# Optimization experiments

Hardware: AMD Instinct MI355X
Metric: run time of the kernel (lower is better)

Reference implementation:

```python
import jax, jax.numpy as jnp
import numpy as np

N = 50000          # nodes
E = 800000         # edges (avg degree 16)
IN, H, OUT = 128, 256, 128
K = 100            # low-rank attention rank (hard-coded self.k = 100)
BN_EPS = 1e-5


def _lin(key, din, dout):
    return jax.random.normal(key, (din, dout), jnp.float32) / np.sqrt(din)


def setup_inputs() -> dict:
    key = jax.random.key(0)
    ks = jax.random.split(key, 16)
    inp = {
        "x": jax.random.normal(ks[0], (N, IN), jnp.float32),
        "edge_index": jax.random.randint(ks[1], (2, E), 0, N, jnp.int32),
    }
    dins = [IN, H, H]
    douts = [H, H, OUT]
    j = 2
    for i, (di, do) in enumerate(zip(dins, douts)):
        inp[f"cw{i}"] = _lin(ks[j], di, H); j += 1          # GCNConv weight
        inp[f"cb{i}"] = jnp.zeros((H,), jnp.float32)          # GCNConv bias
        inp[f"aw{i}"] = _lin(ks[j], di, 4 * K); j += 1        # attention U|V|Z|T projection
        inp[f"ab{i}"] = jnp.zeros((4 * K,), jnp.float32)
        inp[f"rw{i}"] = _lin(ks[j], 2 * K + H, do); j += 1    # dimension_reduce linear
        inp[f"rb{i}"] = jnp.zeros((do,), jnp.float32)
    for i in range(2):                                        # BN for first num_layers-1 blocks
        inp[f"g{i}"] = jnp.ones((H,), jnp.float32)
        inp[f"bt{i}"] = jnp.zeros((H,), jnp.float32)
    return inp


def _gcn(x, W, b, src, dst):
    n = x.shape[0]
    loops = jnp.arange(n, dtype=src.dtype)
    s = jnp.concatenate([src, loops])
    d = jnp.concatenate([dst, loops])
    deg = jax.ops.segment_sum(jnp.ones(d.shape, x.dtype), d, num_segments=n)
    dis = jax.lax.rsqrt(jnp.maximum(deg, 1.0))  # deg >= 1 due to self loops
    h = x @ W                                    # [N, H]
    msg = h[s] * (dis[s] * dis[d])[:, None]      # [E+N, H]
    return jax.ops.segment_sum(msg, d, num_segments=n) + b


def _lowrank(x, Aw, Ab):
    # LowRankAttention: tmp = relu(x W); split into U,V,Z,T of width K each.
    t = jax.nn.relu(x @ Aw + Ab)                 # [N, 4K]
    U, V, Z, T = t[:, :K], t[:, K:2 * K], t[:, 2 * K:3 * K], t[:, 3 * K:]
    n = x.shape[0]
    # joint_normalize2: scalar norm factor
    nf = jnp.sum(U @ (V.T @ jnp.ones((n, 1), x.dtype))) / n + 1e-6
    res = U @ (V.T @ Z)                          # low-rank global attention [N, K]
    return jnp.concatenate([res / nf, T], axis=1)  # [N, 2K]


def _bn(x, g, b):
    m = jnp.mean(x, axis=0)
    v = jnp.var(x, axis=0)
    return (x - m) * jax.lax.rsqrt(v + BN_EPS) * g + b


def reference(x, edge_index, cw0, cb0, aw0, ab0, rw0, rb0, g0, bt0,
              cw1, cb1, aw1, ab1, rw1, rb1, g1, bt1,
              cw2, cb2, aw2, ab2, rw2, rb2):
    src, dst = edge_index[0], edge_index[1]
    layers = [(cw0, cb0, aw0, ab0, rw0, rb0, g0, bt0),
              (cw1, cb1, aw1, ab1, rw1, rb1, g1, bt1)]
    for cw, cb, aw, ab, rw, rb, g, bt in layers:
        x_local = jax.nn.relu(_gcn(x, cw, cb, src, dst))  # dropout p=0 (eval)
        x_global = _lowrank(x, aw, ab)
        x = jax.nn.relu(jnp.concatenate([x_global, x_local], axis=1) @ rw + rb)
        x = _bn(x, g, bt)
    x_local = jax.nn.relu(_gcn(x, cw2, cb2, src, dst))
    x_global = _lowrank(x, aw2, ab2)
    return jnp.concatenate([x_global, x_local], axis=1) @ rw2 + rb2
```

## Files before the change

### kernel.cpp

```cpp
#include <hip/hip_runtime.h>

typedef _Float16 f16;
typedef __attribute__((ext_vector_type(8))) _Float16 f16x8;
typedef __attribute__((ext_vector_type(4))) _Float16 f16x4;
typedef __attribute__((ext_vector_type(2))) _Float16 f16x2;
typedef __attribute__((ext_vector_type(4))) float f32x4;

__global__ __launch_bounds__(256, 4) void gemm4(
    const f16* __restrict__ A, int lda,
    const f16* __restrict__ Bt, int Kd,
    const float* __restrict__ bias,
    f16* __restrict__ Cb, float* __restrict__ Cf, int ldc,
    int R, int ncols, int relu,
    float* __restrict__ csbuf,
    float* __restrict__ bnsum_ptr,
    f16* __restrict__ hbD, f16* __restrict__ tbufD, f16* __restrict__ xcatD,
    int mode)
{
    __shared__ char smem[36864];
    f16* As = (f16*)smem;
    f16* Bs = (f16*)(smem + 18432);
    float* scr = (float*)(smem + 34816);

    const int tid  = threadIdx.x;
    const int wid  = tid >> 6;
    const int lane = tid & 63;
    const int m    = lane & 15;
    const int quad = lane >> 4;
    const int wr   = wid >> 1;
    const int wc   = wid & 1;

    const long rowblk  = (long)blockIdx.x * 128;
    const int  colbase = blockIdx.y * 128;

    f32x4 acc[4][4];
#pragma unroll
    for (int rt = 0; rt < 4; ++rt)
#pragma unroll
        for (int ct = 0; ct < 4; ++ct)
            acc[rt][ct] = f32x4{0.f, 0.f, 0.f, 0.f};

    for (int k0 = 0; k0 < Kd; k0 += 64) {
        const int BK = (Kd - k0 >= 64) ? 64 : (Kd - k0);
        if (k0) __syncthreads();
        if (BK == 64) {
#pragma unroll
            for (int i = 0; i < 4; ++i) {
                int u = i * 256 + tid;
                int r = u >> 3, s = u & 7;
                long rr = rowblk + r; if (rr > (long)R - 1) rr = (long)R - 1;
                *(f16x8*)&As[r * 72 + s * 8] = *(const f16x8*)(A + rr * (long)lda + k0 + s * 8);
            }
#pragma unroll
            for (int i = 0; i < 4; ++i) {
                int u = i * 256 + tid;
                int c = u >> 3, s = u & 7;
                *(f16x8*)&Bs[c * 72 + s * 8] =
                    *(const f16x8*)(Bt + (long)(colbase + c) * Kd + k0 + s * 8);
            }
        } else {
#pragma unroll
            for (int i = 0; i < 2; ++i) {
                int u = i * 256 + tid;
                int r = u >> 2, s = u & 3;
                long rr = rowblk + r; if (rr > (long)R - 1) rr = (long)R - 1;
                *(f16x8*)&As[r * 72 + s * 8] = *(const f16x8*)(A + rr * (long)lda + k0 + s * 8);
            }
#pragma unroll
            for (int i = 0; i < 2; ++i) {
                int u = i * 256 + tid;
                int c = u >> 2, s = u & 3;
                *(f16x8*)&Bs[c * 72 + s * 8] =
                    *(const f16x8*)(Bt + (long)(colbase + c) * Kd + k0 + s * 8);
            }
        }
        __syncthreads();
#pragma unroll 2
        for (int kk = 0; kk < BK; kk += 32) {
            f16x8 a[4], b[4];
#pragma unroll
            for (int rt = 0; rt < 4; ++rt)
                a[rt] = *(const f16x8*)&As[(wr * 64 + rt * 16 + m) * 72 + kk + quad * 8];
#pragma unroll
            for (int ct = 0; ct < 4; ++ct)
                b[ct] = *(const f16x8*)&Bs[(wc * 64 + ct * 16 + m) * 72 + kk + quad * 8];
#pragma unroll
            for (int ct = 0; ct < 4; ++ct)
#pragma unroll
                for (int rt = 0; rt < 4; ++rt)
                    acc[rt][ct] = __builtin_amdgcn_mfma_f32_16x16x32_f16(a[rt], b[ct], acc[rt][ct], 0, 0, 0);
        }
    }

    __syncthreads();

    if (mode == 0 && Cf) {
#pragma unroll
        for (int ct = 0; ct < 4; ++ct) {
            int col = colbase + wc * 64 + ct * 16 + m;
            if (col >= ncols) continue;
            float bv = bias ? bias[col] : 0.f;
#pragma unroll
            for (int rt = 0; rt < 4; ++rt) {
#pragma unroll
                for (int r = 0; r < 4; ++r) {
                    long row = rowblk + wr * 64 + rt * 16 + quad * 4 + r;
                    if (row < R) {
                        float v = acc[rt][ct][r] + bv;
                        if (relu && v < 0.f) v = 0.f;
                        Cf[row * (long)ldc + col] = v;
                    }
                }
            }
        }
        return;
    }

    float rsum[4], rsq[4];
#pragma unroll
    for (int ct = 0; ct < 4; ++ct) { rsum[ct] = 0.f; rsq[ct] = 0.f; }

    f16* epw = (f16*)smem + wid * (64 * 68);

    const bool needsum = (mode == 1) ? (colbase == 256 || colbase == 384)
                                     : (bnsum_ptr != nullptr);

#pragma unroll
    for (int ct = 0; ct < 4; ++ct) {
        int col = colbase + wc * 64 + ct * 16 + m;
        float bv;
        if (mode == 1) bv = bias[col];
        else           bv = (bias && col < ncols) ? bias[col] : 0.f;
        bool isrelu = (mode == 1) ? (col >= 256) : (relu != 0);
#pragma unroll
        for (int rt = 0; rt < 4; ++rt) {
#pragma unroll
            for (int r = 0; r < 4; ++r) {
                long row = rowblk + wr * 64 + rt * 16 + quad * 4 + r;
                float v = acc[rt][ct][r] + bv;
                if (isrelu && v < 0.f) v = 0.f;
                if (needsum && row < R && col < ((mode == 1) ? 656 : ncols)) {
                    rsum[ct] += v;
                    rsq[ct]  += v * v;
                }
                epw[(rt * 16 + quad * 4 + r) * 68 + ct * 16 + m] = (f16)v;
            }
        }
    }

#pragma unroll
    for (int it = 0; it < 16; ++it) {
        int rl = it * 4 + (lane >> 4);
        int ch = lane & 15;
        long grow = rowblk + wr * 64 + rl;
        if (grow >= R) continue;
        f16x4 vv = *(const f16x4*)&epw[rl * 68 + ch * 4];
        int c4 = colbase + wc * 64 + ch * 4;
        if (mode == 1) {
            f16* dst; int ld2, c2;
            if (c4 < 256)      { dst = hbD;   ld2 = 256; c2 = c4; }
            else if (c4 < 556) { dst = tbufD; ld2 = 300; c2 = c4 - 256; }
            else if (c4 < 656) { dst = xcatD; ld2 = 456; c2 = c4 - 556; }
            else continue;
            *(f16x4*)&dst[grow * (long)ld2 + c2] = vv;
        } else {
            if (c4 < ncols)
                *(f16x4*)&Cb[grow * (long)ldc + c4] = vv;
        }
    }

    if (needsum) {
        __syncthreads();
#pragma unroll
        for (int ct = 0; ct < 4; ++ct) {
            float s = rsum[ct];
            s += __shfl_xor(s, 16);
            s += __shfl_xor(s, 32);
            float q = rsq[ct];
            q += __shfl_xor(q, 16);
            q += __shfl_xor(q, 32);
            if (quad == 0) {
                scr[wr * 128 + wc * 64 + ct * 16 + m]       = s;
                scr[256 + wr * 128 + wc * 64 + ct * 16 + m] = q;
            }
        }
        __syncthreads();
        if (tid < 128) {
            int gcol = colbase + tid;
            float s = scr[tid] + scr[128 + tid];
            if (mode == 1) {
                if (gcol >= 256 && gcol < 456) atomicAdd(&csbuf[gcol - 256], s);
            } else if (gcol < ncols) {
                float q = scr[256 + tid] + scr[384 + tid];
                atomicAdd(&bnsum_ptr[gcol], s);
                atomicAdd(&bnsum_ptr[256 + gcol], q);
            }
        }
    }
}

struct PrepJobs {
    const float* src[13];
    void*        dst[13];
    int   K[13], ncols[13], Kd[13], type[13];
    long  start[13], elems[13];
    int   njobs;
};

__global__ __launch_bounds__(256) void prep_all(PrepJobs J)
{
    long b = blockIdx.x;
    int j = 0;
    for (int i = 1; i < J.njobs; ++i)
        if (b >= J.start[i]) j = i;
    long idx = (b - J.start[j]) * 256 + threadIdx.x;
    if (idx >= J.elems[j]) return;
    int ty = J.type[j];
    if (ty == 0) {
        int Kd = J.Kd[j];
        int k = (int)(idx % Kd);
        long n = idx / Kd;
        float v = (k < J.K[j] && n < J.ncols[j]) ? J.src[j][(long)k * J.ncols[j] + n] : 0.f;
        ((f16*)J.dst[j])[idx] = (f16)v;
    } else if (ty == 1) {
        ((f16*)J.dst[j])[idx] = (f16)J.src[j][idx];
    } else if (ty == 2) {
        ((float*)J.dst[j])[idx] = 0.f;
    } else {
        float v = (idx >= 256 && idx < 656) ? J.src[j][idx - 256] : 0.f;
        ((float*)J.dst[j])[idx] = v;
    }
}

__global__ void hist_kernel(const int* __restrict__ dst, int E, int* __restrict__ cnt)
{
    int e = blockIdx.x * 256 + threadIdx.x;
    if (e < E) atomicAdd(&cnt[dst[e]], 1);
}

__global__ __launch_bounds__(1024) void scanA_kernel(const int* __restrict__ cnt, int n,
                                                     int* __restrict__ csum)
{
    __shared__ int sdata[1024];
    int t = threadIdx.x;
    int i = blockIdx.x * 1024 + t;
    sdata[t] = (i < n) ? cnt[i] : 0;
    __syncthreads();
    for (int d = 512; d > 0; d >>= 1) {
        if (t < d) sdata[t] += sdata[t + d];
        __syncthreads();
    }
    if (t == 0) csum[blockIdx.x] = sdata[0];
}

__global__ void scanB_kernel(int* __restrict__ csum, int nchunks, int n, int* __restrict__ rowptr)
{
    if (threadIdx.x == 0) {
        int run = 0;
        for (int b = 0; b < nchunks; ++b) {
            int v = csum[b];
            csum[b] = run;
            run += v;
        }
        rowptr[n] = run;
    }
}

__global__ __launch_bounds__(1024) void scanC_kernel(const int* __restrict__ cnt, int n,
                                                     const int* __restrict__ csum,
                                                     int* __restrict__ rowptr,
                                                     int* __restrict__ cursor,
                                                     float* __restrict__ dis)
{
    __shared__ int sdata[1024];
    int t = threadIdx.x;
    int i = blockIdx.x * 1024 + t;
    int v = (i < n) ? cnt[i] : 0;
    sdata[t] = v;
    __syncthreads();
    for (int d = 1; d < 1024; d <<= 1) {
        int x = (t >= d) ? sdata[t - d] : 0;
        __syncthreads();
        sdata[t] += x;
        __syncthreads();
    }
    if (i < n) {
        int excl = csum[blockIdx.x] + sdata[t] - v;
        rowptr[i] = excl;
        cursor[i] = excl;
        dis[i] = rsqrtf((float)(v + 1));
    }
}

__global__ void scatter_kernel(const int* __restrict__ src, const int* __restrict__ dst,
                               int E, int* __restrict__ cursor, int* __restrict__ colidx)
{
    int e = blockIdx.x * 256 + threadIdx.x;
    if (e < E) {
        int d = dst[e];
        int pos = atomicAdd(&cursor[d], 1);
        colidx[pos] = src[e];
    }
}

__global__ __launch_bounds__(256) void agg_kernel(
    const f16* __restrict__ h, const int* __restrict__ rowptr,
    const int* __restrict__ colidx, const float* __restrict__ dis,
    const float* __restrict__ cb, f16* __restrict__ out, int ldc, int R)
{
    int wid = threadIdx.x >> 6, lane = threadIdx.x & 63;
    int i = blockIdx.x * 4 + wid;
    if (i >= R) return;
    float disi = dis[i];
    f16x4 hv = *(const f16x4*)(h + (long)i * 256 + lane * 4);
    float acc[4];
#pragma unroll
    for (int j = 0; j < 4; ++j) acc[j] = (float)hv[j] * disi;
    int e0 = rowptr[i], e1 = rowptr[i + 1];
    int e = e0;
    for (; e + 3 < e1; e += 4) {
        int s0 = colidx[e], s1 = colidx[e + 1], s2 = colidx[e + 2], s3 = colidx[e + 3];
        float w0 = dis[s0], w1 = dis[s1], w2 = dis[s2], w3 = dis[s3];
        f16x4 h0 = *(const f16x4*)(h + (long)s0 * 256 + lane * 4);
        f16x4 h1 = *(const f16x4*)(h + (long)s1 * 256 + lane * 4);
        f16x4 h2 = *(const f16x4*)(h + (long)s2 * 256 + lane * 4);
        f16x4 h3 = *(const f16x4*)(h + (long)s3 * 256 + lane * 4);
#pragma unroll
        for (int j = 0; j < 4; ++j)
            acc[j] += (float)h0[j] * w0 + (float)h1[j] * w1
                    + (float)h2[j] * w2 + (float)h3[j] * w3;
    }
    for (; e < e1; ++e) {
        int s = colidx[e];
        float w = dis[s];
        f16x4 hs = *(const f16x4*)(h + (long)s * 256 + lane * 4);
#pragma unroll
        for (int j = 0; j < 4; ++j) acc[j] += (float)hs[j] * w;
    }
    f16x4 o;
#pragma unroll
    for (int j = 0; j < 4; ++j) {
        float v = acc[j] * disi + cb[lane * 4 + j];
        if (v < 0.f) v = 0.f;
        o[j] = (f16)v;
    }
    *(f16x4*)(out + (long)i * ldc + lane * 4) = o;
}

#define VTZ_BLOCKS 192
__global__ __launch_bounds__(256) void vtz_mfma(const f16* __restrict__ t, int ld, int R,
                                                float* __restrict__ Mpart)
{
    __shared__ f16 Vt[112 * 72];
    __shared__ f16 Zt[112 * 72];
    const int tid  = threadIdx.x;
    const int wid  = tid >> 6;
    const int lane = tid & 63;
    const int m    = lane & 15;
    const int quad = lane >> 4;

    for (int idx = tid; idx < 12 * 64; idx += 256) {
        int c = 100 + (idx >> 6), r = idx & 63;
        Vt[c * 72 + r] = (f16)0.f;
        Zt[c * 72 + r] = (f16)0.f;
    }

    f32x4 acc[2][7];
#pragma unroll
    for (int rt = 0; rt < 2; ++rt)
#pragma unroll
        for (int ct = 0; ct < 7; ++ct)
            acc[rt][ct] = f32x4{0.f, 0.f, 0.f, 0.f};

    for (long base = (long)blockIdx.x * 64; base < R; base += (long)gridDim.x * 64) {
        __syncthreads();
        for (int idx = tid; idx < 50 * 64; idx += 256) {
            int r = idx / 50, c2 = (idx - r * 50) * 2;
            f16x2 v2 = f16x2{(f16)0.f, (f16)0.f};
            f16x2 z2 = f16x2{(f16)0.f, (f16)0.f};
            if (base + r < R) {
                v2 = *(const f16x2*)(t + (base + r) * ld + 100 + c2);
                z2 = *(const f16x2*)(t + (base + r) * ld + 200 + c2);
            }
            Vt[c2 * 72 + r] = v2[0]; Vt[(c2 + 1) * 72 + r] = v2[1];
            Zt[c2 * 72 + r] = z2[0]; Zt[(c2 + 1) * 72 + r] = z2[1];
        }
        __syncthreads();
#pragma unroll
        for (int ks = 0; ks < 2; ++ks) {
            int k0 = ks * 32 + quad * 8;
            f16x8 b[7];
#pragma unroll
            for (int ct = 0; ct < 7; ++ct)
                b[ct] = *(const f16x8*)&Zt[(ct * 16 + m) * 72 + k0];
#pragma unroll
            for (int rt = 0; rt < 2; ++rt) {
                int tr = wid + rt * 4;
                if (tr >= 7) continue;
                f16x8 a = *(const f16x8*)&Vt[(tr * 16 + m) * 72 + k0];
#pragma unroll
                for (int ct = 0; ct < 7; ++ct)
                    acc[rt][ct] = __builtin_amdgcn_mfma_f32_16x16x32_f16(a, b[ct], acc[rt][ct], 0, 0, 0);
            }
        }
    }

    float* out = Mpart + (long)blockIdx.x * 10000;
#pragma unroll
    for (int rt = 0; rt < 2; ++rt) {
        int tr = wid + rt * 4;
        if (tr >= 7) continue;
#pragma unroll
        for (int ct = 0; ct < 7; ++ct) {
            int b = ct * 16 + m;
            if (b >= 100) continue;
#pragma unroll
            for (int r = 0; r < 4; ++r) {
                int a = tr * 16 + quad * 4 + r;
                if (a < 100) out[a * 100 + b] = acc[rt][ct][r];
            }
        }
    }
}

__global__ __launch_bounds__(256) void vtz_reduce2(const float* __restrict__ Mpart,
                                                   f16* __restrict__ MT,
                                                   const float* __restrict__ cs, int R)
{
    __shared__ float s2[256];
    int t = threadIdx.x;
    float v = (t < 100) ? cs[t] * cs[100 + t] : 0.f;
    s2[t] = v;
    __syncthreads();
    for (int d = 128; d > 0; d >>= 1) {
        if (t < d) s2[t] += s2[t + d];
        __syncthreads();
    }
    float scale = 1.0f / (s2[0] / (float)R + 1e-6f);

    int idx = blockIdx.x * 256 + t;
    if (idx >= 10000) return;
    float s = 0.f;
    for (int b = 0; b < VTZ_BLOCKS; ++b) s += Mpart[(long)b * 10000 + idx];
    s *= scale;
    int a = idx / 100, c = idx - a * 100;
    MT[c * 128 + a] = (f16)s;
}

__global__ __launch_bounds__(256) void bn_fold2(
    f16* __restrict__ bigBT,
    const float* __restrict__ cwf, const float* __restrict__ awf,
    const float* __restrict__ bnsum, const float* __restrict__ g,
    const float* __restrict__ bt, int R,
    const float* __restrict__ ab0, float* __restrict__ biascat)
{
    __shared__ float a_s[256], b_s[256];
    const int t = threadIdx.x;
    {
        float s0 = bnsum[t];
        float s1 = bnsum[256 + t];
        float mean = s0 / (float)R;
        float var  = s1 / (float)R - mean * mean;
        if (var < 0.f) var = 0.f;
        float a = g[t] * rsqrtf(var + 1e-5f);
        a_s[t] = a;
        b_s[t] = bt[t] - mean * a;
    }
    __syncthreads();
    const int bid = blockIdx.x;
    if (bid < 768) {
        long idx = (long)bid * 256 + t;
        bigBT[idx] = (f16)((float)bigBT[idx] * a_s[t]);
    } else if (bid == 768) {
        float s = 0.f;
        for (int k = 0; k < 256; ++k) s += b_s[k] * cwf[(long)k * 256 + t];
        biascat[t] = s;
    } else {
        int n = (bid - 769) * 256 + t;
        if (n < 400) {
            float s = ab0[n];
            for (int k = 0; k < 256; ++k) s += b_s[k] * awf[(long)k * 400 + n];
            biascat[256 + n] = s;
        }
    }
}

extern "C" void kernel_launch(void* const* d_in, const int* in_sizes, int n_in,
                              void* d_out, int out_size, void* d_ws, size_t ws_size,
                              hipStream_t stream)
{
    (void)n_in; (void)out_size; (void)ws_size;
    const int N = in_sizes[0] / 128;
    const int E = in_sizes[1] / 2;

    const float* x0 = (const float*)d_in[0];
    const int*  ei   = (const int*)d_in[1];
    const int*  esrc = ei;
    const int*  edst = ei + E;
    const float *cw[3], *cbv[3], *aw[3], *abv[3], *rw[3], *rbv[3];
    for (int l = 0; l < 3; ++l) {
        cw[l]  = (const float*)d_in[2 + 6 * l];
        cbv[l] = (const float*)d_in[3 + 6 * l];
        aw[l]  = (const float*)d_in[4 + 6 * l];
        abv[l] = (const float*)d_in[5 + 6 * l];
        rw[l]  = (const float*)d_in[6 + 6 * l];
        rbv[l] = (const float*)d_in[7 + 6 * l];
    }
    const float* g[2]   = {(const float*)d_in[20], (const float*)d_in[22]};
    const float* btb[2] = {(const float*)d_in[21], (const float*)d_in[23]};

    char* p = (char*)d_ws;
    auto carve = [&](size_t bytes) -> char* {
        char* r = p; p += (bytes + 255) & ~(size_t)255; return r;
    };
    int*   cnt    = (int*)carve((size_t)N * 4);
    int*   rowptr = (int*)carve((size_t)(N + 1) * 4);
    int*   cursor = (int*)carve((size_t)N * 4);
    int*   colidx = (int*)carve((size_t)E * 4);
    float* dis    = (float*)carve((size_t)N * 4);
    int*   csum   = (int*)carve(256 * 4);
    float* Mpart  = (float*)carve((size_t)VTZ_BLOCKS * 10000 * 4);
    float* zr     = (float*)carve(9984 * 4);
    float* csbufL[3] = {zr, zr + 256, zr + 512};
    float* bnsumA = zr + 768;
    float* bnsumB = zr + 1280;
    f16*   MT     = (f16*)(zr + 1792);
    float* biascat = (float*)carve(768 * 4);
    f16*   bigBT[3], *rwT[3];
    int din[3] = {128, 256, 256};
    int dou[3] = {256, 256, 128};
    for (int l = 0; l < 3; ++l) {
        bigBT[l] = (f16*)carve((size_t)768 * din[l] * 2);
        rwT[l]   = (f16*)carve((size_t)dou[l] * 480 * 2);
    }
    f16*   xbf  = (f16*)carve((size_t)N * 256 * 2);
    float* hbuf = (float*)carve((size_t)N * 256 * 4);
    f16*   hb   = (f16*)hbuf;
    f16*   tbuf = (f16*)carve((size_t)N * 300 * 2);
    f16*   xcat = (f16*)carve(((size_t)N * 456 + 32) * 2);

    PrepJobs J{};
    int nj = 0; long blk = 0;
    auto addJob = [&](const float* s, void* d, int K, int nc, int Kd, int ty, long elems) {
        J.src[nj] = s; J.dst[nj] = d; J.K[nj] = K; J.ncols[nj] = nc; J.Kd[nj] = Kd;
        J.type[nj] = ty; J.start[nj] = blk; J.elems[nj] = elems;
        blk += (elems + 255) / 256; ++nj;
    };
    for (int l = 0; l < 3; ++l)
        addJob(cw[l], bigBT[l], din[l], 256, din[l], 0, (long)256 * din[l]);
    for (int l = 0; l < 3; ++l)
        addJob(aw[l], bigBT[l] + (long)256 * din[l], din[l], 400, din[l], 0, (long)512 * din[l]);
    for (int l = 0; l < 3; ++l)
        addJob(rw[l], rwT[l], 456, dou[l], 480, 0, (long)dou[l] * 480);
    addJob(x0, xbf, 0, 0, 0, 1, (long)N * 128);
    addJob(nullptr, zr, 0, 0, 0, 2, 9984);
    addJob(nullptr, cnt, 0, 0, 0, 2, N);
    addJob(abv[0], biascat, 0, 0, 0, 3, 768);
    J.njobs = nj;

    prep_all<<<(unsigned)blk, 256, 0, stream>>>(J);

    const int nchunks = (N + 1023) / 1024;
    hist_kernel<<<(E + 255) / 256, 256, 0, stream>>>(edst, E, cnt);
    scanA_kernel<<<nchunks, 1024, 0, stream>>>(cnt, N, csum);
    scanB_kernel<<<1, 64, 0, stream>>>(csum, nchunks, N, rowptr);
    scanC_kernel<<<nchunks, 1024, 0, stream>>>(cnt, N, csum, rowptr, cursor, dis);
    scatter_kernel<<<(E + 255) / 256, 256, 0, stream>>>(esrc, edst, E, cursor, colidx);

    int lda = 128;
    const unsigned gx = (unsigned)((N + 127) / 128);

    for (int l = 0; l < 3; ++l) {
        float* bnsumX = (l == 0) ? bnsumA : bnsumB;

        gemm4<<<dim3(gx, 6), 256, 0, stream>>>(xbf, lda, bigBT[l], din[l], biascat,
                                               nullptr, nullptr, 0, N, 656, 0,
                                               csbufL[l], nullptr,
                                               hb, tbuf, xcat + 100, 1);
        vtz_mfma<<<VTZ_BLOCKS, 256, 0, stream>>>(tbuf, 300, N, Mpart);
        vtz_reduce2<<<40, 256, 0, stream>>>(Mpart, MT, csbufL[l], N);
        gemm4<<<dim3(gx, 1), 256, 0, stream>>>(tbuf, 300, MT, 128, nullptr,
                                               xcat, nullptr, 456, N, 100, 0,
                                               nullptr, nullptr,
                                               nullptr, nullptr, nullptr, 0);
        agg_kernel<<<(N + 3) / 4, 256, 0, stream>>>(hb, rowptr, colidx, dis, cbv[l],
                                                    xcat + 200, 456, N);
        if (l < 2) {
            gemm4<<<dim3(gx, 2), 256, 0, stream>>>(xcat, 456, rwT[l], 480, rbv[l],
                                                   xbf, nullptr, 256, N, 256, 1,
                                                   nullptr, bnsumX,
                                                   nullptr, nullptr, nullptr, 0);
            bn_fold2<<<771, 256, 0, stream>>>(bigBT[l + 1], cw[l + 1], aw[l + 1],
                                              bnsumX, g[l], btb[l], N,
                                              abv[l + 1], biascat);
            lda = 256;
        } else {
            gemm4<<<dim3(gx, 1), 256, 0, stream>>>(xcat, 456, rwT[l], 480, rbv[l],
                                                   nullptr, (float*)d_out, 128, N, 128, 0,
                                                   nullptr, nullptr,
                                                   nullptr, nullptr, nullptr, 0);
        }
    }
}
```

Baseline: 947.8 us.

## Fold low-rank attention product into reduce weights and fuse dual-pass GEMM

Precomputes WU = (V^T Z scaled) @ rw[:100] in a small kernel, so the per-node U@M result never has to be materialized. The reduce GEMM now runs two K-passes: tbuf(U part) times WUT, then xcat2 (T|local) times the remaining rw rows. This removes one full N-row GEMM launch and its write/read of xcat, and pads strides to 320/384 so the partial-tile K path can be dropped. The cost is extra K work in the reduce GEMM, a new pad-zeroing prep job, and a change in the order of fp16 rounding.

```diff
diff --git a/kernel.cpp b/kernel.cpp
--- a/kernel.cpp
+++ b/kernel.cpp
@@ -6,9 +6,9 @@
 typedef __attribute__((ext_vector_type(2))) _Float16 f16x2;
 typedef __attribute__((ext_vector_type(4))) float f32x4;
 
-__global__ __launch_bounds__(256, 4) void gemm4(
-    const f16* __restrict__ A, int lda,
-    const f16* __restrict__ Bt, int Kd,
+__global__ __launch_bounds__(256, 4) void gemm5(
+    const f16* __restrict__ A, int lda, const f16* __restrict__ Bt, int Kd,
+    const f16* __restrict__ A2, int lda2, const f16* __restrict__ Bt2, int Kd2,
     const float* __restrict__ bias,
     f16* __restrict__ Cb, float* __restrict__ Cf, int ldc,
     int R, int ncols, int relu,
@@ -40,55 +40,43 @@
         for (int ct = 0; ct < 4; ++ct)
             acc[rt][ct] = f32x4{0.f, 0.f, 0.f, 0.f};
 
-    for (int k0 = 0; k0 < Kd; k0 += 64) {
-        const int BK = (Kd - k0 >= 64) ? 64 : (Kd - k0);
-        if (k0) __syncthreads();
-        if (BK == 64) {
+    for (int pass = 0; pass < 2; ++pass) {
+        const f16* Ap; const f16* Bp; int ldap, Kdp;
+        if (pass == 0) { Ap = A;  Bp = Bt;  ldap = lda;  Kdp = Kd;  }
+        else           { Ap = A2; Bp = Bt2; ldap = lda2; Kdp = Kd2; }
+        if (!Ap) break;
+        for (int k0 = 0; k0 < Kdp; k0 += 64) {
+            if (pass || k0) __syncthreads();
 #pragma unroll
             for (int i = 0; i < 4; ++i) {
                 int u = i * 256 + tid;
                 int r = u >> 3, s = u & 7;
                 long rr = rowblk + r; if (rr > (long)R - 1) rr = (long)R - 1;
-                *(f16x8*)&As[r * 72 + s * 8] = *(const f16x8*)(A + rr * (long)lda + k0 + s * 8);
+                *(f16x8*)&As[r * 72 + s * 8] = *(const f16x8*)(Ap + rr * (long)ldap + k0 + s * 8);
             }
 #pragma unroll
             for (int i = 0; i < 4; ++i) {
                 int u = i * 256 + tid;
                 int c = u >> 3, s = u & 7;
                 *(f16x8*)&Bs[c * 72 + s * 8] =
-                    *(const f16x8*)(Bt + (long)(colbase + c) * Kd + k0 + s * 8);
-            }
-        } else {
-#pragma unroll
-            for (int i = 0; i < 2; ++i) {
-                int u = i * 256 + tid;
-                int r = u >> 2, s = u & 3;
-                long rr = rowblk + r; if (rr > (long)R - 1) rr = (long)R - 1;
-                *(f16x8*)&As[r * 72 + s * 8] = *(const f16x8*)(A + rr * (long)lda + k0 + s * 8);
-            }
-#pragma unroll
-            for (int i = 0; i < 2; ++i) {
-                int u = i * 256 + tid;
-                int c = u >> 2, s = u & 3;
-                *(f16x8*)&Bs[c * 72 + s * 8] =
-                    *(const f16x8*)(Bt + (long)(colbase + c) * Kd + k0 + s * 8);
-            }
-        }
-        __syncthreads();
+                    *(const f16x8*)(Bp + (long)(colbase + c) * Kdp + k0 + s * 8);
+            }
+            __syncthreads();
 #pragma unroll 2
-        for (int kk = 0; kk < BK; kk += 32) {
-            f16x8 a[4], b[4];
-#pragma unroll
-            for (int rt = 0; rt < 4; ++rt)
-                a[rt] = *(const f16x8*)&As[(wr * 64 + rt * 16 + m) * 72 + kk + quad * 8];
-#pragma unroll
-            for (int ct = 0; ct < 4; ++ct)
-                b[ct] = *(const f16x8*)&Bs[(wc * 64 + ct * 16 + m) * 72 + kk + quad * 8];
-#pragma unroll
-            for (int ct = 0; ct < 4; ++ct)
+            for (int kk = 0; kk < 64; kk += 32) {
+                f16x8 a[4], b[4];
 #pragma unroll
                 for (int rt = 0; rt < 4; ++rt)
-                    acc[rt][ct] = __builtin_amdgcn_mfma_f32_16x16x32_f16(a[rt], b[ct], acc[rt][ct], 0, 0, 0);
+                    a[rt] = *(const f16x8*)&As[(wr * 64 + rt * 16 + m) * 72 + kk + quad * 8];
+#pragma unroll
+                for (int ct = 0; ct < 4; ++ct)
+                    b[ct] = *(const f16x8*)&Bs[(wc * 64 + ct * 16 + m) * 72 + kk + quad * 8];
+#pragma unroll
+                for (int ct = 0; ct < 4; ++ct)
+#pragma unroll
+                    for (int rt = 0; rt < 4; ++rt)
+                        acc[rt][ct] = __builtin_amdgcn_mfma_f32_16x16x32_f16(a[rt], b[ct], acc[rt][ct], 0, 0, 0);
+            }
         }
     }
 
@@ -159,8 +147,8 @@
         if (mode == 1) {
             f16* dst; int ld2, c2;
             if (c4 < 256)      { dst = hbD;   ld2 = 256; c2 = c4; }
-            else if (c4 < 556) { dst = tbufD; ld2 = 300; c2 = c4 - 256; }
-            else if (c4 < 656) { dst = xcatD; ld2 = 456; c2 = c4 - 556; }
+            else if (c4 < 556) { dst = tbufD; ld2 = 320; c2 = c4 - 256; }
+            else if (c4 < 656) { dst = xcatD; ld2 = 384; c2 = c4 - 556; }
             else continue;
             *(f16x4*)&dst[grow * (long)ld2 + c2] = vv;
         } else {
@@ -199,11 +187,27 @@
     }
 }
 
+__global__ __launch_bounds__(256) void wu_kernel(const f16* __restrict__ MT,
+                                                 const float* __restrict__ rwf, int dou,
+                                                 f16* __restrict__ WUT)
+{
+    int idx = blockIdx.x * 256 + threadIdx.x;
+    if (idx >= (dou << 7)) return;
+    int a = idx & 127, d = idx >> 7;
+    float s = 0.f;
+    if (a < 100) {
+#pragma unroll 4
+        for (int c = 0; c < 100; ++c)
+            s += (float)MT[c * 128 + a] * rwf[(long)c * dou + d];
+    }
+    WUT[d * 128 + a] = (f16)s;
+}
+
 struct PrepJobs {
-    const float* src[13];
-    void*        dst[13];
-    int   K[13], ncols[13], Kd[13], type[13];
-    long  start[13], elems[13];
+    const float* src[16];
+    void*        dst[16];
+    int   K[16], ncols[16], Kd[16], type[16];
+    long  start[16], elems[16];
     int   njobs;
 };
 
@@ -226,9 +230,14 @@
         ((f16*)J.dst[j])[idx] = (f16)J.src[j][idx];
     } else if (ty == 2) {
         ((float*)J.dst[j])[idx] = 0.f;
-    } else {
+    } else if (ty == 3) {
         float v = (idx >= 256 && idx < 656) ? J.src[j][idx - 256] : 0.f;
         ((float*)J.dst[j])[idx] = v;
+    } else {
+        int w = J.Kd[j];
+        long row = idx / w;
+        int col = J.ncols[j] + (int)(idx % w);
+        ((f16*)J.dst[j])[row * J.K[j] + col] = (f16)0.f;
     }
 }
 
@@ -526,18 +535,18 @@
     float* bnsumB = zr + 1280;
     f16*   MT     = (f16*)(zr + 1792);
     float* biascat = (float*)carve(768 * 4);
-    f16*   bigBT[3], *rwT[3];
+    f16*   WUT    = (f16*)carve(256 * 128 * 2);
+    f16*   bigBT[3], *rwT2[3];
     int din[3] = {128, 256, 256};
     int dou[3] = {256, 256, 128};
     for (int l = 0; l < 3; ++l) {
         bigBT[l] = (f16*)carve((size_t)768 * din[l] * 2);
-        rwT[l]   = (f16*)carve((size_t)dou[l] * 480 * 2);
+        rwT2[l]  = (f16*)carve((size_t)dou[l] * 384 * 2);
     }
     f16*   xbf  = (f16*)carve((size_t)N * 256 * 2);
-    float* hbuf = (float*)carve((size_t)N * 256 * 4);
-    f16*   hb   = (f16*)hbuf;
-    f16*   tbuf = (f16*)carve((size_t)N * 300 * 2);
-    f16*   xcat = (f16*)carve(((size_t)N * 456 + 32) * 2);
+    f16*   hb   = (f16*)carve((size_t)N * 256 * 2);
+    f16*   tbuf = (f16*)carve((size_t)N * 320 * 2);
+    f16*   xcat2 = (f16*)carve(((size_t)N * 384 + 64) * 2);
 
     PrepJobs J{};
     int nj = 0; long blk = 0;
@@ -551,11 +560,12 @@
     for (int l = 0; l < 3; ++l)
         addJob(aw[l], bigBT[l] + (long)256 * din[l], din[l], 400, din[l], 0, (long)512 * din[l]);
     for (int l = 0; l < 3; ++l)
-        addJob(rw[l], rwT[l], 456, dou[l], 480, 0, (long)dou[l] * 480);
+        addJob(rw[l] + (long)100 * dou[l], rwT2[l], 356, dou[l], 384, 0, (long)dou[l] * 384);
     addJob(x0, xbf, 0, 0, 0, 1, (long)N * 128);
     addJob(nullptr, zr, 0, 0, 0, 2, 9984);
     addJob(nullptr, cnt, 0, 0, 0, 2, N);
     addJob(abv[0], biascat, 0, 0, 0, 3, 768);
+    addJob(nullptr, xcat2, 384, 356, 28, 4, (long)N * 28);
     J.njobs = nj;
 
     prep_all<<<(unsigned)blk, 256, 0, stream>>>(J);
@@ -573,20 +583,21 @@
     for (int l = 0; l < 3; ++l) {
         float* bnsumX = (l == 0) ? bnsumA : bnsumB;
 
-        gemm4<<<dim3(gx, 6), 256, 0, stream>>>(xbf, lda, bigBT[l], din[l], biascat,
+        gemm5<<<dim3(gx, 6), 256, 0, stream>>>(xbf, lda, bigBT[l], din[l],
+                                               nullptr, 0, nullptr, 0,
+                                               biascat,
                                                nullptr, nullptr, 0, N, 656, 0,
                                                csbufL[l], nullptr,
-                                               hb, tbuf, xcat + 100, 1);
-        vtz_mfma<<<VTZ_BLOCKS, 256, 0, stream>>>(tbuf, 300, N, Mpart);
+                                               hb, tbuf, xcat2, 1);
+        vtz_mfma<<<VTZ_BLOCKS, 256, 0, stream>>>(tbuf, 320, N, Mpart);
         vtz_reduce2<<<40, 256, 0, stream>>>(Mpart, MT, csbufL[l], N);
-        gemm4<<<dim3(gx, 1), 256, 0, stream>>>(tbuf, 300, MT, 128, nullptr,
-                                               xcat, nullptr, 456, N, 100, 0,
-                                               nullptr, nullptr,
-                                               nullptr, nullptr, nullptr, 0);
+        wu_kernel<<<(dou[l] * 128 + 255) / 256, 256, 0, stream>>>(MT, rw[l], dou[l], WUT);
         agg_kernel<<<(N + 3) / 4, 256, 0, stream>>>(hb, rowptr, colidx, dis, cbv[l],
-                                                    xcat + 200, 456, N);
+                                                    xcat2 + 100, 384, N);
         if (l < 2) {
-            gemm4<<<dim3(gx, 2), 256, 0, stream>>>(xcat, 456, rwT[l], 480, rbv[l],
+            gemm5<<<dim3(gx, 2), 256, 0, stream>>>(tbuf, 320, WUT, 128,
+                                                   xcat2, 384, rwT2[l], 384,
+                                                   rbv[l],
                                                    xbf, nullptr, 256, N, 256, 1,
                                                    nullptr, bnsumX,
                                                    nullptr, nullptr, nullptr, 0);
@@ -595,7 +606,9 @@
                                               abv[l + 1], biascat);
             lda = 256;
         } else {
-            gemm4<<<dim3(gx, 1), 256, 0, stream>>>(xcat, 456, rwT[l], 480, rbv[l],
+            gemm5<<<dim3(gx, 1), 256, 0, stream>>>(tbuf, 320, WUT, 128,
+                                                   xcat2, 384, rwT2[l], 384,
+                                                   rbv[l],
                                                    nullptr, (float*)d_out, 128, N, 128, 0,
                                                    nullptr, nullptr,
                                                    nullptr, nullptr, nullptr, 0);
```

New measurement: 888.9 us. 6.2% less time.
